# Performance work log

Hardware: AMD Instinct MI355X
Metric: run time of the kernel (lower is better)

Reference implementation:

```python
import jax, jax.numpy as jnp
import numpy as np

HIDDEN = 1024
N_HEAD = 16
HEAD_DIM = HIDDEN // N_HEAD  # 64
BATCH = 1
SEQ = 4096
THETA = 10000.0


def _rope_cos_sin(seq_len, head_dim, dtype=jnp.float32):
    # freqs[t, j] = t / theta^(2j/dim), j in [0, dim/2)
    inv_freq = 1.0 / (THETA ** (jnp.arange(0, head_dim, 2, dtype=dtype) / head_dim))
    t = jnp.arange(seq_len, dtype=dtype)
    freqs = jnp.outer(t, inv_freq)           # [S, D/2]
    return jnp.cos(freqs), jnp.sin(freqs)


def _apply_rope(x, cos, sin):
    # x: [B, S, H, D]; pairs (x[...,2j], x[...,2j+1]) rotated by angle freqs[t, j]
    x2 = x.reshape(*x.shape[:-1], -1, 2)       # [B, S, H, D/2, 2]
    x_re, x_im = x2[..., 0], x2[..., 1]
    c = cos[None, :, None, :]                   # [1, S, 1, D/2]
    s = sin[None, :, None, :]
    out_re = x_re * c - x_im * s
    out_im = x_re * s + x_im * c
    out = jnp.stack([out_re, out_im], axis=-1)  # [B, S, H, D/2, 2]
    return out.reshape(x.shape)


def setup_inputs() -> dict:
    key = jax.random.key(0)
    kx, kq, kk, kv = jax.random.split(key, 4)
    scale = 1.0 / np.sqrt(HIDDEN)
    return {
        "x": jax.random.normal(kx, (BATCH, SEQ, HIDDEN), dtype=jnp.float32),
        "wq": jax.random.normal(kq, (HIDDEN, HIDDEN), dtype=jnp.float32) * scale,
        "wk": jax.random.normal(kk, (HIDDEN, HIDDEN), dtype=jnp.float32) * scale,
        "wv": jax.random.normal(kv, (HIDDEN, HIDDEN), dtype=jnp.float32) * scale,
    }


def reference(x, wq, wk, wv):
    B, S, _ = x.shape
    # torch nn.Linear(no bias): y = x @ W.T
    xq = (x @ wq.T).reshape(B, S, N_HEAD, HEAD_DIM).astype(jnp.float32)
    xk = (x @ wk.T).reshape(B, S, N_HEAD, HEAD_DIM).astype(jnp.float32)
    xv = (x @ wv.T).reshape(B, S, N_HEAD, HEAD_DIM).astype(jnp.float32)

    cos, sin = _rope_cos_sin(S, HEAD_DIM)
    q = _apply_rope(xq, cos, sin)
    k = _apply_rope(xk, cos, sin)

    # [B, H, S, S] scores, no causal mask (matches source)
    scores = jnp.einsum("bqhd,bkhd->bhqk", q, k) / jnp.sqrt(
        jnp.asarray(HEAD_DIM, dtype=q.dtype))
    attn = jax.nn.softmax(scores, axis=-1)
    out = jnp.einsum("bhqk,bkhd->bqhd", attn, xv)  # [B, S, H, D]
    return out.reshape(B, S, N_HEAD * HEAD_DIM)
```

## Files before the change

kernel.cpp:

```cpp
#include <hip/hip_runtime.h>
#include <stdint.h>


#define SEQLEN 4096
#define NHEAD 16
#define HDIM 64

typedef __bf16 bf16x8 __attribute__((ext_vector_type(8)));
typedef float f32x4 __attribute__((ext_vector_type(4)));
typedef float f32x16 __attribute__((ext_vector_type(16)));

__device__ __forceinline__ unsigned short f2bf(float f) {
  union { float f; unsigned int u; } v; v.f = f;
  unsigned int r = v.u + 0x7FFFu + ((v.u >> 16) & 1u);
  return (unsigned short)(r >> 16);
}
__device__ __forceinline__ unsigned int pkc(float lo, float hi) {
  union { __bf16 b[2]; unsigned int u; } z;
  z.b[0] = (__bf16)lo; z.b[1] = (__bf16)hi;
  return z.u;
}
__device__ __forceinline__ bf16x8 as_bf(uint4 v) { return __builtin_bit_cast(bf16x8, v); }
__device__ __forceinline__ f32x4 mfma16(bf16x8 a, bf16x8 b, f32x4 c) {
  return __builtin_amdgcn_mfma_f32_16x16x32_bf16(a, b, c, 0, 0, 0);
}
__device__ __forceinline__ f32x16 mfma32(bf16x8 a, bf16x8 b, f32x16 c) {
  return __builtin_amdgcn_mfma_f32_32x32x16_bf16(a, b, c, 0, 0, 0);
}
__device__ __forceinline__ void gll16(const void* g, void* l) {
  __builtin_amdgcn_global_load_lds(
      (const __attribute__((address_space(1))) void*)g,
      (__attribute__((address_space(3))) void*)l, 16, 0, 0);
}

__global__ __launch_bounds__(256) void k_prep(
    const float* __restrict__ x, const float* __restrict__ wq,
    const float* __restrict__ wk, const float* __restrict__ wv,
    unsigned short* __restrict__ xbf, unsigned short* __restrict__ wbf,
    float2* __restrict__ ctst) {
  const int NX = SEQLEN * 1024 / 4;
  const int NW = 1024 * 1024 / 4;
  if (blockIdx.x < 7168) {
    int i = blockIdx.x * 256 + threadIdx.x;
    float4 v;
    unsigned short* dst;
    int di;
    if (i < NX) {
      v = ((const float4*)x)[i]; dst = xbf; di = i;
    } else {
      int j = i - NX;
      const float4* src = (const float4*)((j < NW) ? wq : (j < 2 * NW) ? wk : wv);
      v = src[j & (NW - 1)];
      dst = wbf; di = j;
    }
    ushort4 o; o.x = f2bf(v.x); o.y = f2bf(v.y); o.z = f2bf(v.z); o.w = f2bf(v.w);
    ((ushort4*)dst)[di] = o;
  } else {
    int i = (blockIdx.x - 7168) * 256 + threadIdx.x;
    int s = i >> 5, j = i & 31;
    double inv = exp(-(double)j * 0.28782313662425572);
    double a = (double)s * inv;
    float2 cs; cs.x = (float)cos(a); cs.y = (float)sin(a);
    ctst[i] = cs;
  }
}

__global__ __launch_bounds__(256) void k_gemm(
    const unsigned short* __restrict__ xbf, const unsigned short* __restrict__ wbf,
    const float2* __restrict__ ctst,
    unsigned short* __restrict__ qbf, unsigned short* __restrict__ Kswz,
    unsigned short* __restrict__ Vswz) {
  __shared__ __align__(16) unsigned short As[2][128 * 32];
  __shared__ __align__(16) unsigned short Bs[2][128 * 32];
  const int t = threadIdx.x;
  const int bn = blockIdx.x, bm = blockIdx.y;
  const int lane = t & 63, wave = t >> 6;
  const int r = lane & 15, g = lane >> 4;
  const int wm = wave >> 1, wn = wave & 1;

  const int c0 = 2 * wave, c1 = 2 * wave + 1;
  const int srowA = lane >> 2, sb = (lane & 3) * 16;
  const char* gA0 = (const char*)xbf + (size_t)(bm * 128 + 16 * c0 + srowA) * 2048 + sb;
  const char* gA1 = (const char*)xbf + (size_t)(bm * 128 + 16 * c1 + srowA) * 2048 + sb;
  const char* gB0 = (const char*)wbf + (size_t)(bn * 128 + 16 * c0 + srowA) * 2048 + sb;
  const char* gB1 = (const char*)wbf + (size_t)(bn * 128 + 16 * c1 + srowA) * 2048 + sb;

  gll16(gA0, (char*)As[0] + c0 * 1024);
  gll16(gA1, (char*)As[0] + c1 * 1024);
  gll16(gB0, (char*)Bs[0] + c0 * 1024);
  gll16(gB1, (char*)Bs[0] + c1 * 1024);
  gA0 += 64; gA1 += 64; gB0 += 64; gB1 += 64;

  f32x4 zero4 = {0.f, 0.f, 0.f, 0.f};
  f32x4 acc[4][4];
#pragma unroll
  for (int m = 0; m < 4; ++m)
#pragma unroll
    for (int n = 0; n < 4; ++n) acc[m][n] = zero4;

  for (int kk = 0; kk < 32; ++kk) {
    __syncthreads();
    if (kk < 31) {
      char* Ad = (char*)As[(kk + 1) & 1];
      char* Bd = (char*)Bs[(kk + 1) & 1];
      gll16(gA0, Ad + c0 * 1024);
      gll16(gA1, Ad + c1 * 1024);
      gll16(gB0, Bd + c0 * 1024);
      gll16(gB1, Bd + c1 * 1024);
      gA0 += 64; gA1 += 64; gB0 += 64; gB1 += 64;
    }
    const char* Ac = (const char*)As[kk & 1];
    const char* Bc = (const char*)Bs[kk & 1];
    bf16x8 af[4], bfr[4];
#pragma unroll
    for (int m = 0; m < 4; ++m)
      af[m] = as_bf(*(const uint4*)(Ac + (wm * 64 + m * 16 + r) * 64 + g * 16));
#pragma unroll
    for (int n = 0; n < 4; ++n)
      bfr[n] = as_bf(*(const uint4*)(Bc + (wn * 64 + n * 16 + r) * 64 + g * 16));
#pragma unroll
    for (int m = 0; m < 4; ++m)
#pragma unroll
      for (int n = 0; n < 4; ++n)
        acc[m][n] = mfma16(af[m], bfr[n], acc[m][n]);
  }

  const int matid = bn >> 3;
#pragma unroll
  for (int m = 0; m < 4; ++m) {
    const int row0 = bm * 128 + wm * 64 + m * 16 + 4 * g;
#pragma unroll
    for (int n = 0; n < 4; ++n) {
      const int col = bn * 128 + wn * 64 + n * 16 + r;
      const int d = col & 63;
      const int hh = (col >> 6) & 15;
      if (matid < 2) {
        const int jdx = (col >> 1) & 31;
        const float sgn = (col & 1) ? 1.0f : -1.0f;
        const float qs = (matid == 0) ? 0.18033688011112042f : 1.0f;
#pragma unroll
        for (int j = 0; j < 4; ++j) {
          float v = acc[m][n][j];
          float p = __shfl_xor(v, 1);
          int key = row0 + j;
          float2 cs = ctst[key * 32 + jdx];
          float o = (v * cs.x + p * cs.y * sgn) * qs;
          if (matid == 0) {
            qbf[(size_t)key * 1024 + (hh * 64 + d)] = f2bf(o);
          } else {
            size_t off = (size_t)hh * 524288 + (size_t)key * 128 +
                         (size_t)((2 * d) ^ ((key & 15) << 3));
            *(unsigned short*)((char*)Kswz + off) = f2bf(o);
          }
        }
      } else {
        ushort4 o;
        o.x = f2bf(acc[m][n][0]); o.y = f2bf(acc[m][n][1]);
        o.z = f2bf(acc[m][n][2]); o.w = f2bf(acc[m][n][3]);
        size_t off = (size_t)hh * 524288 + (size_t)(row0 >> 5) * 4096 +
                     (size_t)(d & 31) * 128 +
                     (size_t)((((d >> 5) * 8 + ((row0 >> 2) & 7)) ^ (d & 15)) << 3);
        *(ushort4*)((char*)Vswz + off) = o;
      }
    }
  }
}

__global__ __launch_bounds__(512) void k_attn(
    const unsigned short* __restrict__ qbf, const unsigned short* __restrict__ Kswz,
    const unsigned short* __restrict__ Vswz, float* __restrict__ out) {
  __shared__ __align__(16) char smem[33280];
  const int t = threadIdx.x;
  const int b = blockIdx.x;
  const int work = (b & 7) * 64 + (b >> 3);
  const int h = work >> 5;
  const int qb = work & 31;
  const int lane = t & 63, wave = t >> 6;
  const int qw = wave & 3, hf = wave >> 2;
  const int li = lane & 31, hi = lane >> 5;
  const int q0 = qb * 128 + qw * 32;
  const int HB = hf * 16384;

  bf16x8 qf[4];
#pragma unroll
  for (int c = 0; c < 4; ++c)
    qf[c] = as_bf(*(const uint4*)((const char*)qbf +
              (size_t)(q0 + li) * 2048 + h * 128 + c * 32 + hi * 16));

  f32x16 z16 = {0.f};
  f32x16 acc[2];
  acc[0] = z16; acc[1] = z16;
  float l4[4] = {0.f, 0.f, 0.f, 0.f};

  const int mmK = (li & 15) ^ (hi << 1);
  int kra[4];
#pragma unroll
  for (int c = 0; c < 4; ++c)
    kra[c] = HB + li * 128 + ((((4 * c) ^ mmK)) << 3);
  const int mmV = (li & 15) ^ hi;
  int vra[2][2];
#pragma unroll
  for (int dt = 0; dt < 2; ++dt)
#pragma unroll
    for (int kc = 0; kc < 2; ++kc)
      vra[dt][kc] = HB + 8192 + li * 128 + ((((dt * 8 + 4 * kc) ^ mmV)) << 3);

  const char* pK = (const char*)Kswz + (size_t)h * 524288 + (size_t)hf * 262144 +
                   (size_t)qw * 1024 + (size_t)lane * 16;
  const char* pV = (const char*)Vswz + (size_t)h * 524288 + (size_t)hf * 262144 +
                   (size_t)qw * 1024 + (size_t)lane * 16;
  char* dK = smem + HB + qw * 1024;
  char* dV = smem + HB + 8192 + qw * 1024;

  gll16(pK, dK);
  gll16(pV, dV);
  pK += 4096; pV += 4096;

  for (int j = 0; j < 64; ++j) {
    __syncthreads();
    if (j < 63) {
      const int NB = ((j + 1) & 1) * 4096;
      gll16(pK, dK + NB);
      gll16(pV, dV + NB);
      pK += 4096; pV += 4096;
    }
    const int JB = (j & 1) * 4096;

    f32x16 sT = z16;
    __builtin_amdgcn_s_setprio(1);
#pragma unroll
    for (int c = 0; c < 4; ++c) {
      uint2 a0 = *(const uint2*)(smem + (kra[c] + JB));
      uint2 a1 = *(const uint2*)(smem + ((kra[c] ^ 8) + JB));
      uint4 ku; ku.x = a0.x; ku.y = a0.y; ku.z = a1.x; ku.w = a1.y;
      sT = mfma32(as_bf(ku), qf[c], sT);
    }
    __builtin_amdgcn_s_setprio(0);

    bf16x8 vf[2][2];
#pragma unroll
    for (int dt = 0; dt < 2; ++dt)
#pragma unroll
      for (int kc = 0; kc < 2; ++kc) {
        uint2 lo = *(const uint2*)(smem + (vra[dt][kc] + JB));
        uint2 hi2 = *(const uint2*)(smem + ((vra[dt][kc] ^ 16) + JB));
        uint4 vv; vv.x = lo.x; vv.y = lo.y; vv.z = hi2.x; vv.w = hi2.y;
        vf[dt][kc] = as_bf(vv);
      }

#pragma unroll
    for (int i = 0; i < 16; ++i) sT[i] = __builtin_amdgcn_exp2f(sT[i]);

#pragma unroll
    for (int i = 0; i < 4; ++i)
      l4[i] += (sT[i] + sT[i + 4]) + (sT[i + 8] + sT[i + 12]);

    bf16x8 pfr[2];
#pragma unroll
    for (int kc = 0; kc < 2; ++kc) {
      const int bix = kc * 8;
      uint4 bw;
      bw.x = pkc(sT[bix + 0], sT[bix + 1]);
      bw.y = pkc(sT[bix + 2], sT[bix + 3]);
      bw.z = pkc(sT[bix + 4], sT[bix + 5]);
      bw.w = pkc(sT[bix + 6], sT[bix + 7]);
      pfr[kc] = as_bf(bw);
    }
    __builtin_amdgcn_s_setprio(1);
#pragma unroll
    for (int kc = 0; kc < 2; ++kc) {
      acc[0] = mfma32(vf[0][kc], pfr[kc], acc[0]);
      acc[1] = mfma32(vf[1][kc], pfr[kc], acc[1]);
    }
    __builtin_amdgcn_s_setprio(0);
  }

  float lrun = (l4[0] + l4[1]) + (l4[2] + l4[3]);
  float lhalf = lrun + __shfl_xor(lrun, 32);

  __syncthreads();
  float* shm = (float*)smem;
  if (hf == 1) {
    float* ab = shm + qw * 2048;
#pragma unroll
    for (int dt = 0; dt < 2; ++dt)
#pragma unroll
      for (int i = 0; i < 16; ++i) {
        int d = (i & 3) + 8 * (i >> 2) + 4 * hi + 32 * dt;
        ab[d * 32 + li] = acc[dt][i];
      }
    if (hi == 0) shm[8192 + qw * 32 + li] = lhalf;
  }
  __syncthreads();
  if (hf == 0) {
    float* ab = shm + qw * 2048;
    float l1 = shm[8192 + qw * 32 + li];
    float linv = 1.0f / (lhalf + l1);
#pragma unroll
    for (int dt = 0; dt < 2; ++dt)
#pragma unroll
      for (int i = 0; i < 16; ++i) {
        int d = (i & 3) + 8 * (i >> 2) + 4 * hi + 32 * dt;
        acc[dt][i] = (acc[dt][i] + ab[d * 32 + li]) * linv;
      }
    __asm__ volatile("" ::: "memory");

    float* eb = shm + qw * 2048;
#pragma unroll
    for (int dt = 0; dt < 2; ++dt) {
#pragma unroll
      for (int i = 0; i < 16; ++i)
        eb[li * 33 + ((i & 3) + 8 * (i >> 2) + 4 * hi)] = acc[dt][i];
      __asm__ volatile("" ::: "memory");
#pragma unroll
      for (int it = 0; it < 16; ++it) {
        int q = it * 2 + hi;
        float v = eb[q * 33 + li];
        out[(size_t)(q0 + q) * 1024 + h * 64 + dt * 32 + li] = v;
      }
      __asm__ volatile("" ::: "memory");
    }
  }
}

extern "C" void kernel_launch(void* const* d_in, const int* in_sizes, int n_in,
                              void* d_out, int out_size, void* d_ws, size_t ws_size,
                              hipStream_t stream) {
  const float* x  = (const float*)d_in[0];
  const float* wq = (const float*)d_in[1];
  const float* wk = (const float*)d_in[2];
  const float* wv = (const float*)d_in[3];
  float* out = (float*)d_out;
  char* ws = (char*)d_ws;

  unsigned short* qbf  = (unsigned short*)(ws);
  unsigned short* Kswz = (unsigned short*)(ws + ((size_t)8 << 20));
  unsigned short* Vswz = (unsigned short*)(ws + ((size_t)16 << 20));
  unsigned short* xbf  = (unsigned short*)(ws + ((size_t)24 << 20));
  unsigned short* wbf  = (unsigned short*)(ws + ((size_t)32 << 20));
  float2* ctst = (float2*)(ws + ((size_t)38 << 20));

  k_prep<<<dim3(7680), dim3(256), 0, stream>>>(x, wq, wk, wv, xbf, wbf, ctst);
  k_gemm<<<dim3(24, 32), dim3(256), 0, stream>>>(xbf, wbf, ctst, qbf, Kswz, Vswz);
  k_attn<<<dim3(512), dim3(512), 0, stream>>>(qbf, Kswz, Vswz, out);
}
```

Before: 154.7 us.

## Write K and V contiguously from GEMM, swizzle in a separate kernel

The GEMM epilogue now stores K row-major and V transposed with plain contiguous stores instead of scattered swizzled stores. A new k_swz kernel rearranges them into the swizzled layouts that the attention kernel expects, and reuses the xbf/wbf workspace regions as output. The aim is to avoid scattered 2-byte stores in the GEMM epilogue, at the cost of an extra kernel launch and an extra read and write pass over K and V.

```diff
diff --git a/kernel.cpp b/kernel.cpp
--- a/kernel.cpp
+++ b/kernel.cpp
@@ -68,8 +68,8 @@
 __global__ __launch_bounds__(256) void k_gemm(
     const unsigned short* __restrict__ xbf, const unsigned short* __restrict__ wbf,
     const float2* __restrict__ ctst,
-    unsigned short* __restrict__ qbf, unsigned short* __restrict__ Kswz,
-    unsigned short* __restrict__ Vswz) {
+    unsigned short* __restrict__ qbf, unsigned short* __restrict__ kbf,
+    unsigned short* __restrict__ vT) {
   __shared__ __align__(16) unsigned short As[2][128 * 32];
   __shared__ __align__(16) unsigned short Bs[2][128 * 32];
   const int t = threadIdx.x;
@@ -137,32 +137,45 @@
       if (matid < 2) {
         const int jdx = (col >> 1) & 31;
         const float sgn = (col & 1) ? 1.0f : -1.0f;
+        unsigned short* dst = (matid == 0) ? qbf : kbf;
         const float qs = (matid == 0) ? 0.18033688011112042f : 1.0f;
 #pragma unroll
         for (int j = 0; j < 4; ++j) {
           float v = acc[m][n][j];
           float p = __shfl_xor(v, 1);
-          int key = row0 + j;
-          float2 cs = ctst[key * 32 + jdx];
+          int srow = row0 + j;
+          float2 cs = ctst[srow * 32 + jdx];
           float o = (v * cs.x + p * cs.y * sgn) * qs;
-          if (matid == 0) {
-            qbf[(size_t)key * 1024 + (hh * 64 + d)] = f2bf(o);
-          } else {
-            size_t off = (size_t)hh * 524288 + (size_t)key * 128 +
-                         (size_t)((2 * d) ^ ((key & 15) << 3));
-            *(unsigned short*)((char*)Kswz + off) = f2bf(o);
-          }
+          dst[(size_t)srow * 1024 + (hh * 64 + d)] = f2bf(o);
         }
       } else {
         ushort4 o;
         o.x = f2bf(acc[m][n][0]); o.y = f2bf(acc[m][n][1]);
         o.z = f2bf(acc[m][n][2]); o.w = f2bf(acc[m][n][3]);
-        size_t off = (size_t)hh * 524288 + (size_t)(row0 >> 5) * 4096 +
-                     (size_t)(d & 31) * 128 +
-                     (size_t)((((d >> 5) * 8 + ((row0 >> 2) & 7)) ^ (d & 15)) << 3);
-        *(ushort4*)((char*)Vswz + off) = o;
-      }
-    }
+        *(ushort4*)&vT[((size_t)(hh * 64 + d)) * SEQLEN + row0] = o;
+      }
+    }
+  }
+}
+
+__global__ __launch_bounds__(256) void k_swz(
+    const unsigned short* __restrict__ kbf, const unsigned short* __restrict__ vT,
+    unsigned long long* __restrict__ Kswz, unsigned long long* __restrict__ Vswz) {
+  const int e = (blockIdx.x & 4095) * 256 + threadIdx.x;
+  if (blockIdx.x < 4096) {
+    const int s = e & 15, key = (e >> 4) & 4095, h = e >> 16;
+    const int os = s ^ (key & 15);
+    unsigned long long v = *(const unsigned long long*)
+        ((const char*)kbf + (size_t)key * 2048 + h * 128 + os * 8);
+    Kswz[((size_t)h << 16) | ((size_t)key << 4) | s] = v;
+  } else {
+    const int s = e & 15, vr = (e >> 4) & 31, kt = (e >> 9) & 127, h = e >> 16;
+    const int os = s ^ (vr & 15);
+    const int d = (os >> 3) * 32 + vr;
+    const int key4 = kt * 32 + (os & 7) * 4;
+    unsigned long long v = *(const unsigned long long*)
+        ((const char*)vT + ((size_t)(h * 64 + d)) * 8192 + key4 * 2);
+    Vswz[((size_t)h << 16) | ((size_t)kt << 9) | ((size_t)vr << 4) | s] = v;
   }
 }
 
@@ -333,14 +346,18 @@
   float* out = (float*)d_out;
   char* ws = (char*)d_ws;
 
-  unsigned short* qbf  = (unsigned short*)(ws);
-  unsigned short* Kswz = (unsigned short*)(ws + ((size_t)8 << 20));
-  unsigned short* Vswz = (unsigned short*)(ws + ((size_t)16 << 20));
-  unsigned short* xbf  = (unsigned short*)(ws + ((size_t)24 << 20));
-  unsigned short* wbf  = (unsigned short*)(ws + ((size_t)32 << 20));
+  unsigned short* qbf = (unsigned short*)(ws);
+  unsigned short* kbf = (unsigned short*)(ws + ((size_t)8 << 20));
+  unsigned short* vT  = (unsigned short*)(ws + ((size_t)16 << 20));
+  unsigned short* xbf = (unsigned short*)(ws + ((size_t)24 << 20));
+  unsigned short* wbf = (unsigned short*)(ws + ((size_t)32 << 20));
   float2* ctst = (float2*)(ws + ((size_t)38 << 20));
+  unsigned long long* Kswz = (unsigned long long*)(ws + ((size_t)24 << 20));
+  unsigned long long* Vswz = (unsigned long long*)(ws + ((size_t)32 << 20));
 
   k_prep<<<dim3(7680), dim3(256), 0, stream>>>(x, wq, wk, wv, xbf, wbf, ctst);
-  k_gemm<<<dim3(24, 32), dim3(256), 0, stream>>>(xbf, wbf, ctst, qbf, Kswz, Vswz);
-  k_attn<<<dim3(512), dim3(512), 0, stream>>>(qbf, Kswz, Vswz, out);
-}
+  k_gemm<<<dim3(24, 32), dim3(256), 0, stream>>>(xbf, wbf, ctst, qbf, kbf, vT);
+  k_swz<<<dim3(8192), dim3(256), 0, stream>>>(kbf, vT, Kswz, Vswz);
+  k_attn<<<dim3(512), dim3(512), 0, stream>>>(qbf, (const unsigned short*)Kswz,
+                                              (const unsigned short*)Vswz, out);
+}
```

Result: no change. 153.7 us (-0.6%).
